# Kernel optimization log

Measured on AMD Instinct MI355X. Metric: run time of the kernel, lower is better.

## Reference

```python
import jax, jax.numpy as jnp
import numpy as np
import math

B, F, S, D, NH, L, DFF, M = 8, 48, 64, 512, 8, 4, 2048, 64
PERIOD = 30
NEG = -1e9
EPS = 1e-5

def _slopes(n):
    start = 2.0 ** (-2.0 ** -(math.log2(n) - 3))
    return np.array([start * (start ** i) for i in range(n)], dtype=np.float32)

def _biased_mask():  # (NH, F, F): causal mask + periodic ALiBi bias, alibi[i,j] = -((i-j)//period)
    i = np.arange(F)[:, None]; j = np.arange(F)[None, :]
    alibi = -((i - j) // PERIOD).astype(np.float32)
    return jnp.asarray(np.where(j <= i, _slopes(NH)[:, None, None] * alibi, NEG).astype(np.float32))

def _ppe():  # (F, D): periodic sinusoidal positional encoding (period 30)
    pos = np.arange(PERIOD, dtype=np.float32)[:, None]
    div = np.exp(np.arange(0, D, 2, dtype=np.float32) * (-math.log(10000.0) / D))
    pe = np.zeros((PERIOD, D), np.float32)
    pe[:, 0::2] = np.sin(pos * div)
    pe[:, 1::2] = np.cos(pos * div)
    return jnp.asarray(np.tile(pe, (F // PERIOD + 1, 1))[:F])

BIASED_MASK = _biased_mask()
PE = _ppe()
MEM_MASK = jnp.where(jnp.eye(F, dtype=bool), 0.0, NEG)  # enc_dec diagonal mask (frame i <-> content i)

def _ln(x, g, b):
    mu = x.mean(-1, keepdims=True)
    var = ((x - mu) ** 2).mean(-1, keepdims=True)
    return (x - mu) * jax.lax.rsqrt(var + EPS) * g + b

def _mha(q, k, v, in_w, in_b, out_w, out_b, nh, mask=None):
    Bq, Tq, d = q.shape
    Tk = k.shape[1]
    dh = d // nh
    wq, wk, wv = jnp.split(in_w, 3, axis=0)
    bq, bk, bv = jnp.split(in_b, 3, axis=0)
    qh = (q @ wq.T + bq).reshape(Bq, Tq, nh, dh).transpose(0, 2, 1, 3)
    kh = (k @ wk.T + bk).reshape(Bq, Tk, nh, dh).transpose(0, 2, 1, 3)
    vh = (v @ wv.T + bv).reshape(Bq, Tk, nh, dh).transpose(0, 2, 1, 3)
    s = jnp.einsum('bhqd,bhkd->bhqk', qh, kh) / jnp.sqrt(jnp.float32(dh))
    if mask is not None:
        s = s + mask
    o = jnp.einsum('bhqk,bhkd->bhqd', jax.nn.softmax(s, axis=-1), vh)
    return o.transpose(0, 2, 1, 3).reshape(Bq, Tq, d) @ out_w.T + out_b

def setup_inputs():
    key = jax.random.key(0)
    ks = iter(jax.random.split(key, 40))
    r = lambda *sh: jax.random.normal(next(ks), sh, jnp.float32) * 0.02
    return dict(
        content_code=jax.random.normal(next(ks), (B, F, D), jnp.float32),
        style_code=jax.random.normal(next(ks), (B, D), jnp.float32),
        style_hiddens=jax.random.normal(next(ks), (B, S, D), jnp.float32),
        init_state=jax.random.normal(next(ks), (B, M), jnp.float32),
        ca_in_w=r(3 * D, D), ca_in_b=r(3 * D), ca_out_w=r(D, D), ca_out_b=r(D),
        se_w=r(D, 2 * D), se_b=r(D),
        mm_w=r(D, M), mm_b=r(D),
        mmr_w=r(M, D), mmr_b=r(M),
        sa_in_w=r(L, 3 * D, D), sa_in_b=r(L, 3 * D), sa_out_w=r(L, D, D), sa_out_b=r(L, D),
        xa_in_w=r(L, 3 * D, D), xa_in_b=r(L, 3 * D), xa_out_w=r(L, D, D), xa_out_b=r(L, D),
        ff1_w=r(L, DFF, D), ff1_b=r(L, DFF), ff2_w=r(L, D, DFF), ff2_b=r(L, D),
        ln_g=jnp.ones((L, 3, D), jnp.float32), ln_b=jnp.zeros((L, 3, D), jnp.float32),
    )

def _forward(content_code, style_code, style_hiddens, init_state,
             ca_in_w, ca_in_b, ca_out_w, ca_out_b, se_w, se_b,
             mm_w, mm_b, mmr_w, mmr_b,
             sa_in_w, sa_in_b, sa_out_w, sa_out_b,
             xa_in_w, xa_in_b, xa_out_w, xa_out_b,
             ff1_w, ff1_b, ff2_w, ff2_b, ln_g, ln_b):
    style_emb_g = style_code[:, None, :]
    # 1-head cross-attn of each content frame against style hiddens; the torch code
    # computes this one query (frame) at a time, which is mathematically identical.
    sel = _mha(content_code, style_hiddens, style_hiddens,
               ca_in_w, ca_in_b, ca_out_w, ca_out_b, 1)  # (B, F, D)

    def emb_new(feat, i):  # style_emb_map(cat([feat, style_emb_l_i])) + global style
        return (jnp.concatenate([feat, sel[:, i:i + 1]], -1) @ se_w.T + se_b) + style_emb_g

    def decoder(x, mem):  # post-norm TransformerDecoder, relu FFN, eval (no dropout)
        T = x.shape[1]
        tgt = BIASED_MASK[None, :, :T, :T]
        mmask = MEM_MASK[:T][None, None]  # (1,1,T,F)
        for l in range(L):
            x = _ln(x + _mha(x, x, x, sa_in_w[l], sa_in_b[l], sa_out_w[l], sa_out_b[l], NH, tgt),
                    ln_g[l, 0], ln_b[l, 0])
            x = _ln(x + _mha(x, mem, mem, xa_in_w[l], xa_in_b[l], xa_out_w[l], xa_out_b[l], NH, mmask),
                    ln_g[l, 1], ln_b[l, 1])
            h = jax.nn.relu(x @ ff1_w[l].T + ff1_b[l]) @ ff2_w[l].T + ff2_b[l]
            x = _ln(x + h, ln_g[l, 2], ln_b[l, 2])
        return x

    dec_emb = emb_new((init_state @ mm_w.T + mm_b)[:, None], 0)  # (B,1,D)
    dec_out = None
    for i in range(F):
        dec_input = dec_emb + PE[:dec_emb.shape[1]]
        dec_out = decoder(dec_input, content_code) @ mmr_w.T + mmr_b  # (B, i+1, M)
        new = dec_out[:, -1:] @ mm_w.T + mm_b
        dec_emb = jnp.concatenate([dec_emb, emb_new(new, i)], axis=1)
    return dec_out, sel

def reference(content_code, style_code, style_hiddens, init_state,
              ca_in_w, ca_in_b, ca_out_w, ca_out_b, se_w, se_b,
              mm_w, mm_b, mmr_w, mmr_b,
              sa_in_w, sa_in_b, sa_out_w, sa_out_b,
              xa_in_w, xa_in_b, xa_out_w, xa_out_b,
              ff1_w, ff1_b, ff2_w, ff2_b, ln_g, ln_b):
    return _forward(content_code, style_code, style_hiddens, init_state,
                    ca_in_w, ca_in_b, ca_out_w, ca_out_b, se_w, se_b,
                    mm_w, mm_b, mmr_w, mmr_b,
                    sa_in_w, sa_in_b, sa_out_w, sa_out_b,
                    xa_in_w, xa_in_b, xa_out_w, xa_out_b,
                    ff1_w, ff1_b, ff2_w, ff2_b, ln_g, ln_b)
```

## Files before the change

kernel.cpp:

```cpp
#include <hip/hip_runtime.h>
#include <hip/hip_fp16.h>


typedef _Float16 h2 __attribute__((ext_vector_type(2)));
__device__ inline h2 u2h(unsigned u){ union{unsigned u; h2 h;} c; c.u=u; return c.h; }
#if __has_builtin(__builtin_amdgcn_fdot2)
__device__ inline float FDOT2(h2 a, h2 b, float c){ return __builtin_amdgcn_fdot2(a, b, c, false); }
#else
__device__ inline float FDOT2(h2 a, h2 b, float c){
  return fmaf((float)a.y, (float)b.y, fmaf((float)a.x, (float)b.x, c));
}
#endif

__device__ inline float aload(const float* p){
  return __hip_atomic_load(p, __ATOMIC_RELAXED, __HIP_MEMORY_SCOPE_AGENT);
}
__device__ inline void astore(float* p, float v){
  __hip_atomic_store(p, v, __ATOMIC_RELAXED, __HIP_MEMORY_SCOPE_AGENT);
}
__device__ inline float2 aload2(const float* base, int pairIdx){
  union { unsigned long long u; float2 f; } c;
  c.u = __hip_atomic_load((const unsigned long long*)base + pairIdx,
                          __ATOMIC_RELAXED, __HIP_MEMORY_SCOPE_AGENT);
  return c.f;
}

__device__ inline float dot_f16(const ushort* wrow, const ushort* xh, int n){
  const uint4* w4 = (const uint4*)wrow;
  const uint4* x4 = (const uint4*)xh;
  float a0=0.f, a1=0.f, a2=0.f, a3=0.f;
  #pragma unroll 4
  for (int i=0; i<(n>>3); ++i){
    uint4 w = w4[i], x = x4[i];
    a0 = FDOT2(u2h(w.x), u2h(x.x), a0);
    a1 = FDOT2(u2h(w.y), u2h(x.y), a1);
    a2 = FDOT2(u2h(w.z), u2h(x.z), a2);
    a3 = FDOT2(u2h(w.w), u2h(x.w), a3);
  }
  return (a0+a1)+(a2+a3);
}
__device__ inline float dot_f32(const float* wrow, const float* x, int n){
  const float4* w4 = (const float4*)wrow;
  float a0=0.f, a1=0.f, a2=0.f, a3=0.f;
  #pragma unroll 4
  for (int i=0; i<(n>>2); ++i){
    float4 w = w4[i];
    const float* xp = x + i*4;
    a0 = fmaf(w.x, xp[0], a0); a1 = fmaf(w.y, xp[1], a1);
    a2 = fmaf(w.z, xp[2], a2); a3 = fmaf(w.w, xp[3], a3);
  }
  return (a0+a1)+(a2+a3);
}

__global__ void k_transpose(const float* __restrict__ src, float* __restrict__ dst, int R, int C){
  __shared__ float tile[32][33];
  int cb = blockIdx.x*32, rb = blockIdx.y*32;
  int tx = threadIdx.x, ty = threadIdx.y;
  for (int i=ty; i<32; i+=8) tile[i][tx] = src[(size_t)(rb+i)*C + cb+tx];
  __syncthreads();
  for (int i=ty; i<32; i+=8) dst[(size_t)(cb+i)*R + rb+tx] = tile[tx][i];
}

__global__ void k_casthf(const float* __restrict__ s, __half* __restrict__ d, int n){
  int i = blockIdx.x*256 + threadIdx.x;
  if (i < n) d[i] = __float2half(s[i]);
}

__global__ void k_linear(const float* __restrict__ A, int lda,
                         const float* __restrict__ Wt, int ldw,
                         const float* __restrict__ bias,
                         float* __restrict__ C, int ldc,
                         int O, int Din,
                         size_t aStr, size_t wStr, size_t bStr, size_t cStr){
  __shared__ float xs[8*1024];
  __shared__ float red[4096];
  int tid = threadIdx.x;
  int r0 = blockIdx.y*8;
  int z = blockIdx.z;
  const float* Az = A + (size_t)z*aStr;
  const float* Wz = Wt + (size_t)z*wStr;
  const float* Bz = bias ? bias + (size_t)z*bStr : nullptr;
  float* Cz = C + (size_t)z*cStr;
  for (int idx=tid; idx<8*Din; idx+=256){
    int ri = idx / Din, d = idx - ri*Din;
    xs[idx] = Az[(size_t)(r0+ri)*lda + d];
  }
  __syncthreads();
  int op = tid & 63, kp = tid >> 6;
  int o = blockIdx.x*128 + op*2;
  int dq = Din >> 2;
  float a0[8] = {0,0,0,0,0,0,0,0}, a1[8] = {0,0,0,0,0,0,0,0};
  for (int d = kp*dq; d < kp*dq+dq; ++d){
    float2 w = *reinterpret_cast<const float2*>(&Wz[(size_t)d*ldw + o]);
    #pragma unroll
    for (int ri=0; ri<8; ++ri){ float x = xs[ri*Din+d]; a0[ri] += x*w.x; a1[ri] += x*w.y; }
  }
  #pragma unroll
  for (int ri=0; ri<8; ++ri){
    red[((kp*64+op)*8+ri)*2]   = a0[ri];
    red[((kp*64+op)*8+ri)*2+1] = a1[ri];
  }
  __syncthreads();
  for (int idx = tid; idx < 1024; idx += 256){
    int ri = idx >> 7, oc = idx & 127;
    int opp = oc >> 1, c = oc & 1;
    float v = red[((0*64+opp)*8+ri)*2 + c] + red[((1*64+opp)*8+ri)*2 + c]
            + red[((2*64+opp)*8+ri)*2 + c] + red[((3*64+opp)*8+ri)*2 + c];
    int oo = blockIdx.x*128 + oc;
    if (Bz) v += Bz[oo];
    Cz[(size_t)(r0+ri)*ldc + oo] = v;
  }
}

__global__ void k_pe(float* __restrict__ pe){
  int idx = blockIdx.x*256 + threadIdx.x;
  int t = idx >> 9, d = idx & 511;
  int p = t % 30;
  int i2 = d & ~1;
  float div = __expf(-(float)i2 * (9.210340371976184f/512.f));
  float ang = (float)p * div;
  pe[idx] = (d & 1) ? cosf(ang) : sinf(ang);
}

__global__ void k_sel_attn(const float* __restrict__ qh, const float* __restrict__ kh,
                           const float* __restrict__ vh, float* __restrict__ o){
  int bf = blockIdx.x;
  int b  = bf / 48;
  int tid = threadIdx.x;
  __shared__ float qs[512];
  __shared__ float ps[64];
  qs[tid] = qh[(size_t)bf*512 + tid];
  qs[tid+256] = qh[(size_t)bf*512 + tid + 256];
  __syncthreads();
  if (tid < 64){
    const float* kr = kh + (size_t)(b*64+tid)*512;
    float a = 0.f;
    for (int d=0; d<512; ++d) a += qs[d]*kr[d];
    ps[tid] = a * 0.04419417382415922f;
  }
  __syncthreads();
  if (tid == 0){
    float m = -1e30f;
    for (int j=0;j<64;++j) m = fmaxf(m, ps[j]);
    float s = 0.f;
    for (int j=0;j<64;++j){ float e = __expf(ps[j]-m); ps[j]=e; s+=e; }
    float iv = 1.f/s;
    for (int j=0;j<64;++j) ps[j] *= iv;
  }
  __syncthreads();
  float a0=0.f, a1=0.f;
  for (int j=0;j<64;++j){
    const float* vr = vh + (size_t)(b*64+j)*512;
    float pj = ps[j];
    a0 += pj*vr[tid]; a1 += pj*vr[tid+256];
  }
  o[(size_t)bf*512+tid] = a0;
  o[(size_t)bf*512+tid+256] = a1;
}

__global__ void k_cat_tail(const float* __restrict__ sel, float* __restrict__ cat){
  int idx = blockIdx.x*256 + threadIdx.x;
  int b = idx >> 9, d = idx & 511;
  cat[b*1024 + 512 + d] = sel[(size_t)(b*48)*512 + d];
}
__global__ void k_add_style(const float* __restrict__ embt, const float* __restrict__ style,
                            float* __restrict__ emb){
  int idx = blockIdx.x*256 + threadIdx.x;
  int b = idx >> 9, e = idx & 511;
  int slot = ((e & 255) << 1) | (e >> 8);
  emb[b*512 + slot] = embt[idx] + style[idx];
}

struct DP {
  unsigned* fl;
  float* z;
  float* emb;
  const ushort *Wqkv, *Wo, *Wf1, *Wf2;
  const float *xa_c, *pe;
  const float *sa_in_b, *sa_out_b, *ff1_b, *ff2_b;
  const float *mmr_w, *mmr_b, *mm_w, *mm_b, *se_w, *se_b;
  const float *ln_g, *ln_b, *style, *sel;
  float* dec_out;
};

__launch_bounds__(256, 1)
__global__ void k_decode(DP p){
  const int tid = threadIdx.x;
  const int i = blockIdx.x;
  const int role = ((i & 7) << 1) | ((i >> 3) & 1);
  const int b = i >> 4;
  const int h = role >> 1, half = role & 1;
  const float slope = exp2f(-(float)(h+1));

  __shared__ float kc[4*48*65];
  __shared__ float vs[4*48*64];
  __shared__ float xs[512];
  __shared__ float red[512];
  __shared__ float qs[64], ps[64], d64[64];
  __shared__ float ns[512];
  __shared__ float lnred[8];
  __shared__ __align__(16) __half xhh[512];
  __shared__ __align__(16) __half anh[64];
  __shared__ __align__(16) __half hsh[128];

  unsigned* flb = p.fl + (size_t)b*48*9*16;
  float* zb = p.z + (size_t)b*48*8*512;

  auto waitc = [&](int t, int s){
    const unsigned* c = flb + (size_t)(t*9+s)*16;
    while (__hip_atomic_load(c, __ATOMIC_RELAXED, __HIP_MEMORY_SCOPE_AGENT) < 16u)
      __builtin_amdgcn_s_sleep(1);
  };
  auto post = [&](int t, int s){
    __syncthreads();
    if (tid == 0)
      __hip_atomic_fetch_add(flb + (size_t)(t*9+s)*16, 1u,
                             __ATOMIC_RELAXED, __HIP_MEMORY_SCOPE_AGENT);
  };
  auto lnorm = [&](float v0, float v1, const float* g, const float* bb,
                   float* out, __half* oh, float& r0, float& r1){
    float s = v0 + v1, q = v0*v0 + v1*v1;
    #pragma unroll
    for (int off=32; off>0; off>>=1){ s += __shfl_xor(s, off, 64); q += __shfl_xor(q, off, 64); }
    if ((tid & 63) == 0){ lnred[tid>>6] = s; lnred[4+(tid>>6)] = q; }
    __syncthreads();
    s = lnred[0]+lnred[1]+lnred[2]+lnred[3];
    q = lnred[4]+lnred[5]+lnred[6]+lnred[7];
    float mu = s * (1.f/512.f);
    float rs = rsqrtf(q*(1.f/512.f) - mu*mu + 1e-5f);
    r0 = (v0-mu)*rs*g[tid]     + bb[tid];
    r1 = (v1-mu)*rs*g[tid+256] + bb[tid+256];
    if (out){ out[tid] = r0; out[tid+256] = r1; }
    if (oh){ oh[tid] = __float2half(r0); oh[tid+256] = __float2half(r1); }
    __syncthreads();
  };

  for (int t=0; t<48; ++t){
    for (int l=0; l<4; ++l){
      const float* xac = p.xa_c + ((size_t)l*384 + b*48 + t)*512;
      float xa0 = xac[tid], xa1 = xac[tid+256];

      float x0, x1;
      if (l == 0){
        float pe0 = p.pe[t*512+tid], pe1 = p.pe[t*512+tid+256];
        if (t > 0) waitc(t-1, 8);
        float2 e = aload2(p.emb + ((size_t)t*8+b)*512, tid);
        x0 = e.x + pe0; x1 = e.y + pe1;
        xhh[tid]     = __float2half(x0);
        xhh[tid+256] = __float2half(x1);
        __syncthreads();
      } else {
        waitc(t, (l-1)*2+1);
        float2 z = aload2(zb + ((size_t)t*8 + (l-1)*2+1)*512, tid);
        lnorm(z.x, z.y, p.ln_g + ((l-1)*3+2)*512, p.ln_b + ((l-1)*3+2)*512,
              nullptr, xhh, x0, x1);
      }
      if (tid < 192){
        int sec = tid >> 6, dch = tid & 63;
        int row = sec*512 + h*64 + dch;
        float acc = dot_f16(p.Wqkv + ((size_t)l*1536+row)*512, (const ushort*)xhh, 512)
                  + p.sa_in_b[l*1536+row];
        if (sec == 0) qs[dch] = acc;
        else if (sec == 1) kc[(l*48+t)*65 + dch] = acc;
        else vs[(l*48+t)*64 + dch] = acc;
      }
      __syncthreads();
      if (tid < 64){
        float sc = -1e30f;
        if (tid <= t){
          float a = 0.f;
          const float* kr = &kc[(l*48+tid)*65];
          #pragma unroll
          for (int d=0; d<64; ++d) a = fmaf(qs[d], kr[d], a);
          sc = a*0.125f - ((t-tid) >= 30 ? slope : 0.f);
        }
        float m = sc;
        #pragma unroll
        for (int off=32; off>0; off>>=1) m = fmaxf(m, __shfl_xor(m, off, 64));
        float e = (tid <= t) ? __expf(sc-m) : 0.f;
        float s = e;
        #pragma unroll
        for (int off=32; off>0; off>>=1) s += __shfl_xor(s, off, 64);
        ps[tid] = e / s;
      }
      __syncthreads();
      {
        int d = tid & 63, jq = tid >> 6;
        float a = 0.f;
        for (int j=jq*12; j<jq*12+12; ++j)
          if (j <= t) a = fmaf(ps[j], vs[(l*48+j)*64 + d], a);
        red[tid] = a;
      }
      __syncthreads();
      if (tid < 64) anh[tid] = __float2half(red[tid]+red[64+tid]+red[128+tid]+red[192+tid]);
      __syncthreads();
      {
        int o = half*256 + tid;
        float acc = dot_f16(p.Wo + (((size_t)l*512+o)*512 + h*64), (const ushort*)anh, 64);
        if (h == 0) acc += (half ? x1 : x0) + p.sa_out_b[l*512+o];
        unsafeAtomicAdd(zb + ((size_t)t*8 + l*2)*512 + ((tid<<1)|half), acc);
      }
      post(t, l*2);

      waitc(t, l*2);
      float r0, r1;
      {
        float2 z = aload2(zb + ((size_t)t*8 + l*2)*512, tid);
        float w0, w1;
        lnorm(z.x, z.y, p.ln_g + (l*3)*512, p.ln_b + (l*3)*512, nullptr, nullptr, w0, w1);
        float u0 = w0 + xa0, u1 = w1 + xa1;
        lnorm(u0, u1, p.ln_g + (l*3+1)*512, p.ln_b + (l*3+1)*512, nullptr, xhh, r0, r1);
      }
      {
        int oo = tid & 127, hh = tid >> 7;
        int row = role*128 + oo;
        red[tid] = dot_f16(p.Wf1 + ((size_t)l*2048+row)*512 + hh*256,
                           (const ushort*)xhh + hh*256, 256);
      }
      __syncthreads();
      if (tid < 128){
        float v = red[tid] + red[128+tid] + p.ff1_b[l*2048 + role*128 + tid];
        hsh[tid] = __float2half(fmaxf(v, 0.f));
      }
      __syncthreads();
      {
        float a0 = dot_f16(p.Wf2 + ((size_t)l*512+tid)*2048 + role*128, (const ushort*)hsh, 128);
        float a1 = dot_f16(p.Wf2 + ((size_t)l*512+tid+256)*2048 + role*128, (const ushort*)hsh, 128);
        if (role == 0){
          a0 += r0 + p.ff2_b[l*512+tid];
          a1 += r1 + p.ff2_b[l*512+tid+256];
        }
        float* zs = zb + ((size_t)t*8 + l*2+1)*512;
        unsafeAtomicAdd(zs + (tid<<1),     a0);
        unsafeAtomicAdd(zs + (tid<<1) + 1, a1);
      }
      post(t, l*2+1);
    }

    waitc(t, 7);
    {
      float2 z = aload2(zb + ((size_t)t*8 + 7)*512, tid);
      float w0, w1;
      lnorm(z.x, z.y, p.ln_g + 11*512, p.ln_b + 11*512, xs, nullptr, w0, w1);
    }
    {
      int o = tid & 63, kq = tid >> 6;
      red[tid] = dot_f32(p.mmr_w + (size_t)o*512 + kq*128, xs + kq*128, 128);
    }
    __syncthreads();
    if (tid < 64){
      float v = red[tid]+red[64+tid]+red[128+tid]+red[192+tid] + p.mmr_b[tid];
      d64[tid] = v;
      if (role == 0) p.dec_out[((size_t)b*48+t)*64 + tid] = v;
    }
    __syncthreads();
    {
      ns[tid]     = dot_f32(p.mm_w + (size_t)tid*64,       d64, 64) + p.mm_b[tid];
      ns[tid+256] = dot_f32(p.mm_w + (size_t)(tid+256)*64, d64, 64) + p.mm_b[tid+256];
    }
    __syncthreads();
    {
      int oo = tid & 31, part = tid >> 5;
      int o = role*32 + oo;
      float acc;
      if (part < 4)
        acc = dot_f32(p.se_w + (size_t)o*1024 + part*128, ns + part*128, 128);
      else
        acc = dot_f32(p.se_w + (size_t)o*1024 + part*128,
                      p.sel + ((size_t)b*48+t)*512 + (part-4)*128, 128);
      red[tid] = acc;
    }
    __syncthreads();
    if (tid < 32){
      float v = 0.f;
      #pragma unroll
      for (int k8=0; k8<8; ++k8) v += red[k8*32+tid];
      int o = role*32 + tid;
      v += p.se_b[o] + p.style[(size_t)b*512+o];
      int slot = ((o & 255) << 1) | (o >> 8);
      astore(p.emb + ((size_t)(t+1)*8+b)*512 + slot, v);
    }
    post(t, 8);
  }
}

extern "C" void kernel_launch(void* const* d_in, const int* in_sizes, int n_in,
                              void* d_out, int out_size, void* d_ws, size_t ws_size,
                              hipStream_t stream){
  (void)in_sizes; (void)n_in; (void)out_size; (void)ws_size;
  const float* content = (const float*)d_in[0];
  const float* style   = (const float*)d_in[1];
  const float* shid    = (const float*)d_in[2];
  const float* init_st = (const float*)d_in[3];
  const float* ca_in_w = (const float*)d_in[4];
  const float* ca_in_b = (const float*)d_in[5];
  const float* ca_out_w= (const float*)d_in[6];
  const float* ca_out_b= (const float*)d_in[7];
  const float* se_w    = (const float*)d_in[8];
  const float* se_b    = (const float*)d_in[9];
  const float* mm_w    = (const float*)d_in[10];
  const float* mm_b    = (const float*)d_in[11];
  const float* mmr_w   = (const float*)d_in[12];
  const float* mmr_b   = (const float*)d_in[13];
  const float* sa_in_w = (const float*)d_in[14];
  const float* sa_in_b = (const float*)d_in[15];
  const float* sa_out_w= (const float*)d_in[16];
  const float* sa_out_b= (const float*)d_in[17];
  const float* xa_in_w = (const float*)d_in[18];
  const float* xa_in_b = (const float*)d_in[19];
  const float* xa_out_w= (const float*)d_in[20];
  const float* xa_out_b= (const float*)d_in[21];
  const float* ff1_w   = (const float*)d_in[22];
  const float* ff1_b   = (const float*)d_in[23];
  const float* ff2_w   = (const float*)d_in[24];
  const float* ff2_b   = (const float*)d_in[25];
  const float* ln_g    = (const float*)d_in[26];
  const float* ln_b    = (const float*)d_in[27];

  float* out = (float*)d_out;
  float* dec_out = out;
  float* sel = out + 8*48*64;

  char* base = (char*)d_ws;
  size_t cur = 0;
  auto alloc = [&](size_t bytes)->char*{
    char* pt = base + cur;
    cur += (bytes + 255) & ~(size_t)255;
    return pt;
  };
  unsigned* fl  = (unsigned*)alloc((size_t)8*48*9*16*4);
  float* zacc   = (float*)alloc((size_t)8*48*8*512*4);
  float* emb    = (float*)alloc((size_t)49*8*512*4);
  size_t zero_span = cur;
  ushort* WqkvH = (ushort*)alloc((size_t)4*1536*512*2);
  ushort* WoH   = (ushort*)alloc((size_t)4*512*512*2);
  ushort* Wf1H  = (ushort*)alloc((size_t)4*2048*512*2);
  ushort* Wf2H  = (ushort*)alloc((size_t)4*512*2048*2);
  float* Wt_mm    = (float*)alloc((size_t)64*512*4);
  float* Wt_se    = (float*)alloc((size_t)1024*512*4);
  float* Wt_ca_in = (float*)alloc((size_t)512*1536*4);
  float* Wt_ca_out= (float*)alloc((size_t)512*512*4);
  float* Wt_xa_v  = (float*)alloc((size_t)4*512*512*4);
  float* Wt_xa_o  = (float*)alloc((size_t)4*512*512*4);
  float* xa_c  = (float*)alloc((size_t)4*384*512*4);
  float* pe    = (float*)alloc((size_t)48*512*4);
  float* qh    = (float*)alloc((size_t)384*512*4);
  float* khb   = (float*)alloc((size_t)512*512*4);
  float* vhb   = (float*)alloc((size_t)512*512*4);
  float* attno = (float*)alloc((size_t)384*512*4);
  float* xtmp4 = (float*)alloc((size_t)4*384*512*4);
  float* catb  = (float*)alloc((size_t)8*1024*4);
  float* embt  = (float*)alloc((size_t)8*512*4);
  (void)vhb;

  hipMemsetAsync(fl, 0, zero_span, stream);

  dim3 tb(32,8);
  k_casthf<<<(4*1536*512+255)/256, 256, 0, stream>>>(sa_in_w, (__half*)WqkvH, 4*1536*512);
  k_casthf<<<(4*512*512+255)/256, 256, 0, stream>>>(sa_out_w, (__half*)WoH,  4*512*512);
  k_casthf<<<(4*2048*512+255)/256, 256, 0, stream>>>(ff1_w,  (__half*)Wf1H, 4*2048*512);
  k_casthf<<<(4*512*2048+255)/256, 256, 0, stream>>>(ff2_w,  (__half*)Wf2H, 4*512*2048);
  for (int l=0; l<4; ++l){
    k_transpose<<<dim3(16,16), tb, 0, stream>>>(xa_in_w + (size_t)l*1536*512 + (size_t)1024*512, Wt_xa_v + (size_t)l*512*512, 512, 512);
    k_transpose<<<dim3(16,16), tb, 0, stream>>>(xa_out_w + (size_t)l*512*512, Wt_xa_o + (size_t)l*512*512, 512, 512);
  }
  k_transpose<<<dim3(16,48), tb, 0, stream>>>(ca_in_w,  Wt_ca_in, 1536, 512);
  k_transpose<<<dim3(16,16), tb, 0, stream>>>(ca_out_w, Wt_ca_out, 512, 512);
  k_transpose<<<dim3(32,16), tb, 0, stream>>>(se_w,  Wt_se, 512, 1024);
  k_transpose<<<dim3(2,16),  tb, 0, stream>>>(mm_w,  Wt_mm, 512, 64);

  k_pe<<<96, 256, 0, stream>>>(pe);

  k_linear<<<dim3(4,48), 256, 0, stream>>>(content, 512, Wt_ca_in, 1536, ca_in_b, qh, 512, 512, 512, 0,0,0,0);
  k_linear<<<dim3(4,64,2), 256, 0, stream>>>(shid, 512, Wt_ca_in + 512, 1536, ca_in_b + 512, khb, 512, 512, 512,
                                             0, 512, 512, (size_t)512*512);
  k_sel_attn<<<384, 256, 0, stream>>>(qh, khb, vhb, attno);
  k_linear<<<dim3(4,48), 256, 0, stream>>>(attno, 512, Wt_ca_out, 512, ca_out_b, sel, 512, 512, 512, 0,0,0,0);

  k_linear<<<dim3(4,48,4), 256, 0, stream>>>(content, 512, Wt_xa_v, 512, xa_in_b + 1024, xtmp4, 512, 512, 512,
                                             0, (size_t)512*512, 1536, (size_t)384*512);
  k_linear<<<dim3(4,48,4), 256, 0, stream>>>(xtmp4, 512, Wt_xa_o, 512, xa_out_b, xa_c, 512, 512, 512,
                                             (size_t)384*512, (size_t)512*512, 512, (size_t)384*512);

  k_linear<<<dim3(4,1), 256, 0, stream>>>(init_st, 64, Wt_mm, 512, mm_b, catb, 1024, 512, 64, 0,0,0,0);
  k_cat_tail<<<16, 256, 0, stream>>>(sel, catb);
  k_linear<<<dim3(4,1), 256, 0, stream>>>(catb, 1024, Wt_se, 512, se_b, embt, 512, 512, 1024, 0,0,0,0);
  k_add_style<<<16, 256, 0, stream>>>(embt, style, emb);

  DP p;
  p.fl = fl; p.z = zacc; p.emb = emb;
  p.Wqkv = WqkvH; p.Wo = WoH; p.Wf1 = Wf1H; p.Wf2 = Wf2H;
  p.xa_c = xa_c; p.pe = pe;
  p.sa_in_b = sa_in_b; p.sa_out_b = sa_out_b; p.ff1_b = ff1_b; p.ff2_b = ff2_b;
  p.mmr_w = mmr_w; p.mmr_b = mmr_b; p.mm_w = mm_w; p.mm_b = mm_b;
  p.se_w = se_w; p.se_b = se_b; p.ln_g = ln_g; p.ln_b = ln_b;
  p.style = style; p.sel = sel; p.dec_out = dec_out;

  k_decode<<<dim3(128), dim3(256), 0, stream>>>(p);
}
```

Measured before the change: 5.264 ms.

## Double decode block threads to 512 and split dot products across lanes

The persistent decode kernel now runs 512 threads per block instead of 256. Each thread owns one feature element rather than two, so the interleaved pair layout and 64-bit atomic loads are dropped. The QKV, Wo, FF1, mmr and se dot products are split across 2 to 16 lanes and combined with shuffle reductions, shortening the per-thread serial dot length on this latency-bound autoregressive chain. The cost is more shuffle and reduction work and more threads contending on the same barriers and atomics.

```diff
diff --git a/kernel.cpp b/kernel.cpp
--- a/kernel.cpp
+++ b/kernel.cpp
@@ -17,12 +17,6 @@
 }
 __device__ inline void astore(float* p, float v){
   __hip_atomic_store(p, v, __ATOMIC_RELAXED, __HIP_MEMORY_SCOPE_AGENT);
-}
-__device__ inline float2 aload2(const float* base, int pairIdx){
-  union { unsigned long long u; float2 f; } c;
-  c.u = __hip_atomic_load((const unsigned long long*)base + pairIdx,
-                          __ATOMIC_RELAXED, __HIP_MEMORY_SCOPE_AGENT);
-  return c.f;
 }
 
 __device__ inline float dot_f16(const ushort* wrow, const ushort* xh, int n){
@@ -166,9 +160,7 @@
 __global__ void k_add_style(const float* __restrict__ embt, const float* __restrict__ style,
                             float* __restrict__ emb){
   int idx = blockIdx.x*256 + threadIdx.x;
-  int b = idx >> 9, e = idx & 511;
-  int slot = ((e & 255) << 1) | (e >> 8);
-  emb[b*512 + slot] = embt[idx] + style[idx];
+  emb[idx] = embt[idx] + style[idx];
 }
 
 struct DP {
@@ -183,7 +175,7 @@
   float* dec_out;
 };
 
-__launch_bounds__(256, 1)
+__launch_bounds__(512, 2)
 __global__ void k_decode(DP p){
   const int tid = threadIdx.x;
   const int i = blockIdx.x;
@@ -198,7 +190,7 @@
   __shared__ float red[512];
   __shared__ float qs[64], ps[64], d64[64];
   __shared__ float ns[512];
-  __shared__ float lnred[8];
+  __shared__ float lnred[16];
   __shared__ __align__(16) __half xhh[512];
   __shared__ __align__(16) __half anh[64];
   __shared__ __align__(16) __half hsh[128];
@@ -206,10 +198,11 @@
   unsigned* flb = p.fl + (size_t)b*48*9*16;
   float* zb = p.z + (size_t)b*48*8*512;
 
-  auto waitc = [&](int t, int s){
+  auto waitz = [&](int t, int s, const float* src)->float{
     const unsigned* c = flb + (size_t)(t*9+s)*16;
     while (__hip_atomic_load(c, __ATOMIC_RELAXED, __HIP_MEMORY_SCOPE_AGENT) < 16u)
       __builtin_amdgcn_s_sleep(1);
+    return aload(src + tid);
   };
   auto post = [&](int t, int s){
     __syncthreads();
@@ -217,52 +210,55 @@
       __hip_atomic_fetch_add(flb + (size_t)(t*9+s)*16, 1u,
                              __ATOMIC_RELAXED, __HIP_MEMORY_SCOPE_AGENT);
   };
-  auto lnorm = [&](float v0, float v1, const float* g, const float* bb,
-                   float* out, __half* oh, float& r0, float& r1){
-    float s = v0 + v1, q = v0*v0 + v1*v1;
+  auto lnorm = [&](float v, const float* g, const float* bb,
+                   float* out, __half* oh)->float{
+    float s = v, q = v*v;
     #pragma unroll
     for (int off=32; off>0; off>>=1){ s += __shfl_xor(s, off, 64); q += __shfl_xor(q, off, 64); }
-    if ((tid & 63) == 0){ lnred[tid>>6] = s; lnred[4+(tid>>6)] = q; }
+    if ((tid & 63) == 0){ lnred[tid>>6] = s; lnred[8+(tid>>6)] = q; }
     __syncthreads();
-    s = lnred[0]+lnred[1]+lnred[2]+lnred[3];
-    q = lnred[4]+lnred[5]+lnred[6]+lnred[7];
+    s = 0.f; q = 0.f;
+    #pragma unroll
+    for (int w=0; w<8; ++w){ s += lnred[w]; q += lnred[8+w]; }
     float mu = s * (1.f/512.f);
     float rs = rsqrtf(q*(1.f/512.f) - mu*mu + 1e-5f);
-    r0 = (v0-mu)*rs*g[tid]     + bb[tid];
-    r1 = (v1-mu)*rs*g[tid+256] + bb[tid+256];
-    if (out){ out[tid] = r0; out[tid+256] = r1; }
-    if (oh){ oh[tid] = __float2half(r0); oh[tid+256] = __float2half(r1); }
+    float r = (v-mu)*rs*g[tid] + bb[tid];
+    if (out) out[tid] = r;
+    if (oh) oh[tid] = __float2half(r);
     __syncthreads();
+    return r;
   };
 
   for (int t=0; t<48; ++t){
     for (int l=0; l<4; ++l){
       const float* xac = p.xa_c + ((size_t)l*384 + b*48 + t)*512;
-      float xa0 = xac[tid], xa1 = xac[tid+256];
-
-      float x0, x1;
+      float xa = xac[tid];
+
       if (l == 0){
-        float pe0 = p.pe[t*512+tid], pe1 = p.pe[t*512+tid+256];
-        if (t > 0) waitc(t-1, 8);
-        float2 e = aload2(p.emb + ((size_t)t*8+b)*512, tid);
-        x0 = e.x + pe0; x1 = e.y + pe1;
-        xhh[tid]     = __float2half(x0);
-        xhh[tid+256] = __float2half(x1);
+        float pe0 = p.pe[t*512+tid];
+        float e;
+        if (t > 0) e = waitz(t-1, 8, p.emb + ((size_t)t*8+b)*512);
+        else       e = aload(p.emb + ((size_t)t*8+b)*512 + tid);
+        float x = e + pe0;
+        xs[tid] = x; xhh[tid] = __float2half(x);
         __syncthreads();
       } else {
-        waitc(t, (l-1)*2+1);
-        float2 z = aload2(zb + ((size_t)t*8 + (l-1)*2+1)*512, tid);
-        lnorm(z.x, z.y, p.ln_g + ((l-1)*3+2)*512, p.ln_b + ((l-1)*3+2)*512,
-              nullptr, xhh, x0, x1);
-      }
-      if (tid < 192){
-        int sec = tid >> 6, dch = tid & 63;
-        int row = sec*512 + h*64 + dch;
-        float acc = dot_f16(p.Wqkv + ((size_t)l*1536+row)*512, (const ushort*)xhh, 512)
-                  + p.sa_in_b[l*1536+row];
-        if (sec == 0) qs[dch] = acc;
-        else if (sec == 1) kc[(l*48+t)*65 + dch] = acc;
-        else vs[(l*48+t)*64 + dch] = acc;
+        float z = waitz(t, (l-1)*2+1, zb + ((size_t)t*8 + (l-1)*2+1)*512);
+        lnorm(z, p.ln_g + ((l-1)*3+2)*512, p.ln_b + ((l-1)*3+2)*512, xs, xhh);
+      }
+      if (tid < 384){
+        int row = tid >> 1, piece = tid & 1;
+        int sec = row >> 6, dch = row & 63;
+        int wrow = sec*512 + h*64 + dch;
+        float acc = dot_f16(p.Wqkv + ((size_t)l*1536+wrow)*512 + piece*256,
+                            (const ushort*)xhh + piece*256, 256);
+        acc += __shfl_xor(acc, 1, 64);
+        if (piece == 0){
+          acc += p.sa_in_b[l*1536+wrow];
+          if (sec == 0) qs[dch] = acc;
+          else if (sec == 1) kc[(l*48+t)*65 + dch] = acc;
+          else vs[(l*48+t)*64 + dch] = acc;
+        }
       }
       __syncthreads();
       if (tid < 64){
@@ -287,98 +283,86 @@
       {
         int d = tid & 63, jq = tid >> 6;
         float a = 0.f;
-        for (int j=jq*12; j<jq*12+12; ++j)
+        for (int j=jq*6; j<jq*6+6; ++j)
           if (j <= t) a = fmaf(ps[j], vs[(l*48+j)*64 + d], a);
         red[tid] = a;
       }
       __syncthreads();
-      if (tid < 64) anh[tid] = __float2half(red[tid]+red[64+tid]+red[128+tid]+red[192+tid]);
+      if (tid < 64){
+        float a = red[tid]+red[64+tid]+red[128+tid]+red[192+tid]
+                + red[256+tid]+red[320+tid]+red[384+tid]+red[448+tid];
+        anh[tid] = __float2half(a);
+      }
       __syncthreads();
       {
-        int o = half*256 + tid;
-        float acc = dot_f16(p.Wo + (((size_t)l*512+o)*512 + h*64), (const ushort*)anh, 64);
-        if (h == 0) acc += (half ? x1 : x0) + p.sa_out_b[l*512+o];
-        unsafeAtomicAdd(zb + ((size_t)t*8 + l*2)*512 + ((tid<<1)|half), acc);
+        int oi = tid >> 1, piece = tid & 1;
+        int o = half*256 + oi;
+        float acc = dot_f16(p.Wo + (((size_t)l*512+o)*512 + h*64) + piece*32,
+                            (const ushort*)anh + piece*32, 32);
+        acc += __shfl_xor(acc, 1, 64);
+        if (piece == 0){
+          if (h == 0) acc += xs[o] + p.sa_out_b[l*512+o];
+          unsafeAtomicAdd(zb + ((size_t)t*8 + l*2)*512 + o, acc);
+        }
       }
       post(t, l*2);
 
-      waitc(t, l*2);
-      float r0, r1;
+      float r;
       {
-        float2 z = aload2(zb + ((size_t)t*8 + l*2)*512, tid);
-        float w0, w1;
-        lnorm(z.x, z.y, p.ln_g + (l*3)*512, p.ln_b + (l*3)*512, nullptr, nullptr, w0, w1);
-        float u0 = w0 + xa0, u1 = w1 + xa1;
-        lnorm(u0, u1, p.ln_g + (l*3+1)*512, p.ln_b + (l*3+1)*512, nullptr, xhh, r0, r1);
+        float z = waitz(t, l*2, zb + ((size_t)t*8 + l*2)*512);
+        float w = lnorm(z, p.ln_g + (l*3)*512, p.ln_b + (l*3)*512, nullptr, nullptr);
+        float u = w + xa;
+        r = lnorm(u, p.ln_g + (l*3+1)*512, p.ln_b + (l*3+1)*512, nullptr, xhh);
       }
       {
-        int oo = tid & 127, hh = tid >> 7;
-        int row = role*128 + oo;
-        red[tid] = dot_f16(p.Wf1 + ((size_t)l*2048+row)*512 + hh*256,
-                           (const ushort*)xhh + hh*256, 256);
-      }
-      __syncthreads();
-      if (tid < 128){
-        float v = red[tid] + red[128+tid] + p.ff1_b[l*2048 + role*128 + tid];
-        hsh[tid] = __float2half(fmaxf(v, 0.f));
+        int row = tid >> 2, piece = tid & 3;
+        float a = dot_f16(p.Wf1 + ((size_t)l*2048 + role*128 + row)*512 + piece*128,
+                          (const ushort*)xhh + piece*128, 128);
+        a += __shfl_xor(a, 1, 64);
+        a += __shfl_xor(a, 2, 64);
+        if (piece == 0)
+          hsh[row] = __float2half(fmaxf(a + p.ff1_b[l*2048 + role*128 + row], 0.f));
       }
       __syncthreads();
       {
         float a0 = dot_f16(p.Wf2 + ((size_t)l*512+tid)*2048 + role*128, (const ushort*)hsh, 128);
-        float a1 = dot_f16(p.Wf2 + ((size_t)l*512+tid+256)*2048 + role*128, (const ushort*)hsh, 128);
-        if (role == 0){
-          a0 += r0 + p.ff2_b[l*512+tid];
-          a1 += r1 + p.ff2_b[l*512+tid+256];
-        }
-        float* zs = zb + ((size_t)t*8 + l*2+1)*512;
-        unsafeAtomicAdd(zs + (tid<<1),     a0);
-        unsafeAtomicAdd(zs + (tid<<1) + 1, a1);
+        if (role == 0) a0 += r + p.ff2_b[l*512+tid];
+        unsafeAtomicAdd(zb + ((size_t)t*8 + l*2+1)*512 + tid, a0);
       }
       post(t, l*2+1);
     }
 
-    waitc(t, 7);
     {
-      float2 z = aload2(zb + ((size_t)t*8 + 7)*512, tid);
-      float w0, w1;
-      lnorm(z.x, z.y, p.ln_g + 11*512, p.ln_b + 11*512, xs, nullptr, w0, w1);
+      float z = waitz(t, 7, zb + ((size_t)t*8 + 7)*512);
+      lnorm(z, p.ln_g + 11*512, p.ln_b + 11*512, xs, nullptr);
     }
     {
-      int o = tid & 63, kq = tid >> 6;
-      red[tid] = dot_f32(p.mmr_w + (size_t)o*512 + kq*128, xs + kq*128, 128);
+      int o8 = tid >> 3, p8 = tid & 7;
+      float a = dot_f32(p.mmr_w + (size_t)o8*512 + p8*64, xs + p8*64, 64);
+      a += __shfl_xor(a, 1, 64);
+      a += __shfl_xor(a, 2, 64);
+      a += __shfl_xor(a, 4, 64);
+      if (p8 == 0) d64[o8] = a + p.mmr_b[o8];
     }
     __syncthreads();
-    if (tid < 64){
-      float v = red[tid]+red[64+tid]+red[128+tid]+red[192+tid] + p.mmr_b[tid];
-      d64[tid] = v;
-      if (role == 0) p.dec_out[((size_t)b*48+t)*64 + tid] = v;
-    }
+    if (role == 0 && tid < 64) p.dec_out[((size_t)b*48+t)*64 + tid] = d64[tid];
+    ns[tid] = dot_f32(p.mm_w + (size_t)tid*64, d64, 64) + p.mm_b[tid];
     __syncthreads();
     {
-      ns[tid]     = dot_f32(p.mm_w + (size_t)tid*64,       d64, 64) + p.mm_b[tid];
-      ns[tid+256] = dot_f32(p.mm_w + (size_t)(tid+256)*64, d64, 64) + p.mm_b[tid+256];
-    }
-    __syncthreads();
-    {
-      int oo = tid & 31, part = tid >> 5;
-      int o = role*32 + oo;
-      float acc;
-      if (part < 4)
-        acc = dot_f32(p.se_w + (size_t)o*1024 + part*128, ns + part*128, 128);
-      else
-        acc = dot_f32(p.se_w + (size_t)o*1024 + part*128,
-                      p.sel + ((size_t)b*48+t)*512 + (part-4)*128, 128);
-      red[tid] = acc;
-    }
-    __syncthreads();
-    if (tid < 32){
-      float v = 0.f;
-      #pragma unroll
-      for (int k8=0; k8<8; ++k8) v += red[k8*32+tid];
-      int o = role*32 + tid;
-      v += p.se_b[o] + p.style[(size_t)b*512+o];
-      int slot = ((o & 255) << 1) | (o >> 8);
-      astore(p.emb + ((size_t)(t+1)*8+b)*512 + slot, v);
+      int o5 = tid >> 4, p16 = tid & 15;
+      int o = role*32 + o5;
+      float acc = (p16 < 8)
+        ? dot_f32(p.se_w + (size_t)o*1024 + p16*64, ns + p16*64, 64)
+        : dot_f32(p.se_w + (size_t)o*1024 + p16*64,
+                  p.sel + ((size_t)b*48+t)*512 + (p16-8)*64, 64);
+      acc += __shfl_xor(acc, 1, 64);
+      acc += __shfl_xor(acc, 2, 64);
+      acc += __shfl_xor(acc, 4, 64);
+      acc += __shfl_xor(acc, 8, 64);
+      if (p16 == 0){
+        acc += p.se_b[o] + p.style[(size_t)b*512+o];
+        astore(p.emb + ((size_t)(t+1)*8+b)*512 + o, acc);
+      }
     }
     post(t, 8);
   }
@@ -496,5 +480,5 @@
   p.se_w = se_w; p.se_b = se_b; p.ln_g = ln_g; p.ln_b = ln_b;
   p.style = style; p.sel = sel; p.dec_out = dec_out;
 
-  k_decode<<<dim3(128), dim3(256), 0, stream>>>(p);
-}
+  k_decode<<<dim3(128), dim3(512), 0, stream>>>(p);
+}
```

After: 5.122 ms. 2.7% less time.
